# Kernel tuning notes

Measured on AMD Instinct MI355X. Metric: run time of the kernel, lower is better.

## Reference

```python
import jax, jax.numpy as jnp
import numpy as np

# dims: n=batch, T=n_shifts, dX=16, dU=8, H=256 hidden, L=128 ldim, K=64 n_aux (L=2K)

def setup_inputs() -> dict:
    key = jax.random.key(0)
    ks = jax.random.split(key, 16)
    n, T, dX, dU, H, L, K = 64, 64, 16, 8, 256, 128, 64
    def lin(k, fan_in, shape):
        return (jax.random.uniform(k, shape, jnp.float32) * 2.0 - 1.0) / np.sqrt(fan_in)
    xs = jax.random.normal(ks[0], (n, T, dX), jnp.float32)
    us = jax.random.normal(ks[1], (n, T - 1, dU), jnp.float32)
    theta = jax.random.uniform(ks[2], (K,), jnp.float32) * (2.0 * np.pi)
    inp = {
        'xs': xs, 'us': us,
        # stacked x-aux encoders (K copies): BN affine, 3 linear layers (last no bias), output scale
        'x_gamma': jnp.ones((K, dX)), 'x_beta': jnp.zeros((K, dX)),
        'xW1': lin(ks[3], dX, (K, dX, H)), 'xb1': jnp.zeros((K, H)),
        'xW2': lin(ks[4], H, (K, H, H)), 'xb2': jnp.zeros((K, H)),
        'xW3': lin(ks[5], H, (K, H, L)), 'x_scale': jnp.ones((K, L)),
        # stacked u-aux encoders (K copies)
        'u_gamma': jnp.ones((K, dU)), 'u_beta': jnp.zeros((K, dU)),
        'uW1': lin(ks[6], dU, (K, dU, H)), 'ub1': jnp.zeros((K, H)),
        'uW2': lin(ks[7], H, (K, H, H)), 'ub2': jnp.zeros((K, H)),
        'uW3': lin(ks[8], H, (K, H, L)), 'u_scale': jnp.ones((K, L)),
        # Jordan-block complex eigenvalues (|lam| ~ 0.95)
        'reL': 0.95 * jnp.cos(theta), 'imL': 0.95 * jnp.sin(theta),
        # decoder C: Linear(ldim, dim, bias=False) -> weight [dX, L]
        'C_W': lin(ks[9], L, (dX, L)),
    }
    return inp


def _encoder(x, gamma, beta, W1, b1, W2, b2, W3, scale):
    # x: [M, D]; stacked params over K nets. BN stats (training mode) are per-feature over M,
    # identical across nets since the same x feeds every net.
    mu = x.mean(0)
    var = ((x - mu) ** 2).mean(0)
    xn = (x - mu) * jax.lax.rsqrt(var + 1e-5)          # [M, D]
    h = xn[None] * gamma[:, None, :] + beta[:, None, :]  # [K, M, D]
    h = jax.nn.leaky_relu(jnp.einsum('kmd,kdh->kmh', h, W1) + b1[:, None, :])
    h = jax.nn.leaky_relu(jnp.einsum('kmd,kdh->kmh', h, W2) + b2[:, None, :])
    h = jnp.einsum('kmd,kdh->kmh', h, W3)               # last layer: no bias
    return h * scale[:, None, :]                        # [K, M, L]


def reference(xs, us, x_gamma, x_beta, xW1, xb1, xW2, xb2, xW3, x_scale,
              u_gamma, u_beta, uW1, ub1, uW2, ub2, uW3, u_scale, reL, imL, C_W):
    n, T, dX = xs.shape
    K = reL.shape[0]
    L = 2 * K
    Tm1 = T - 1
    # phi1s: [n, T, K(net), K(pair), 2]
    phi = _encoder(xs.reshape(n * T, dX), x_gamma, x_beta, xW1, xb1, xW2, xb2, xW3, x_scale)
    phi1s = jnp.moveaxis(phi, 0, 1).reshape(n, T, K, K, 2)
    # ures = psi(u) - psi(0): [n, T-1, K, K, 2]
    uflat = us.reshape(n * Tm1, -1)
    psi_u = _encoder(uflat, u_gamma, u_beta, uW1, ub1, uW2, ub2, uW3, u_scale)
    psi_0 = _encoder(jnp.zeros_like(uflat), u_gamma, u_beta, uW1, ub1, uW2, ub2, uW3, u_scale)
    ures = jnp.moveaxis(psi_u - psi_0, 0, 1).reshape(n, Tm1, K, K, 2)
    # block-diagonal Koopman: per net j a 2x2 rotation-scale [[re, im], [-im, re]]
    R = jnp.stack([jnp.stack([reL, imL], -1), jnp.stack([-imL, reL], -1)], -2)  # [K, 2, 2]

    def step(p, u_t):
        p = jnp.einsum('bjkc,jcd->bjkd', p + u_t, R)
        return p, p

    _, preds = jax.lax.scan(step, phi1s[:, 0], jnp.moveaxis(ures, 0, 1))
    preds = jnp.moveaxis(preds, 0, 1)  # [n, T-1, K, K, 2]

    def phi2y(p):
        # sum over net axis (-3), flatten pair dims -> [.., L], decode with C
        return p.sum(-3).reshape(*p.shape[:-3], L) @ C_W.T

    y = phi2y(phi1s[:, 1:])
    y_pred = phi2y(preds)
    return y, y_pred
```

## Files before the change

kernel.cpp:

```cpp
#include <hip/hip_runtime.h>

typedef __bf16 bf16_t;
typedef __bf16 bf16x8 __attribute__((ext_vector_type(8)));
typedef __bf16 bf16x4 __attribute__((ext_vector_type(4)));
typedef float  f32x4  __attribute__((ext_vector_type(4)));

__global__ __launch_bounds__(256) void prep_all_kernel(
    const float* __restrict__ xW1, const float* __restrict__ xb1,
    const float* __restrict__ xg,  const float* __restrict__ xbeta,
    const float* __restrict__ uW1, const float* __restrict__ ub1,
    const float* __restrict__ ug,  const float* __restrict__ ubeta,
    const float* __restrict__ xW2, const float* __restrict__ uW2,
    const float* __restrict__ xW3, const float* __restrict__ uW3,
    const float* __restrict__ x_scale, const float* __restrict__ u_scale,
    const float* __restrict__ ub2,
    const float* __restrict__ xs, const float* __restrict__ us,
    bf16_t* __restrict__ xW1t, float* __restrict__ xb1p,
    bf16_t* __restrict__ uW1t, float* __restrict__ ub1p,
    bf16_t* __restrict__ xW2t, bf16_t* __restrict__ uW2t,
    bf16_t* __restrict__ xW3t, bf16_t* __restrict__ uW3t,
    float* __restrict__ psi0, float* __restrict__ part)
{
    const int t = blockIdx.x, tid = threadIdx.x;
    __shared__ float tile[32][65];
    __shared__ float h1[256], h2[256];

    if (t < 6144) {
        const float* in; bf16_t* outp; const float* scale = nullptr;
        int j, r0, c0, C;
        if (t < 4096) {
            C = 256;
            j = (t & 2047) >> 5;
            const int tl = t & 31; r0 = (tl >> 3) * 64; c0 = (tl & 7) * 32;
            if (t < 2048) { in = xW2; outp = xW2t; }
            else          { in = uW2; outp = uW2t; }
        } else {
            C = 128;
            const int l = t - 4096;
            j = (l & 1023) >> 4;
            const int tl = l & 15; r0 = (tl >> 2) * 64; c0 = (tl & 3) * 32;
            if (l < 1024) { in = xW3; outp = xW3t; scale = x_scale + j * 128; }
            else          { in = uW3; outp = uW3t; scale = u_scale + j * 128; }
        }
        in += (size_t)j * 256 * C;
        bf16_t* op = outp + (size_t)j * 256 * C;
        const int cx = tid & 31, ry0 = tid >> 5;
        #pragma unroll
        for (int p = 0; p < 8; p++)
            tile[cx][ry0 + p * 8] = in[(size_t)(r0 + ry0 + p * 8) * C + c0 + cx];
        __syncthreads();
        const int rr = tid & 63, cb = tid >> 6;
        #pragma unroll
        for (int p = 0; p < 8; p++) {
            const int cl = cb + p * 4;
            float sc = scale ? scale[c0 + cl] : 1.f;
            op[(size_t)(c0 + cl) * 256 + r0 + rr] = (bf16_t)(tile[cl][rr] * sc);
        }
    } else if (t < 6272) {
        const int bid = t - 6144, j = bid & 63, h = tid;
        const float *W1, *b1, *gamma, *beta; bf16_t* W1t; float* b1p; int D;
        if (bid < 64) { W1 = xW1; b1 = xb1; gamma = xg; beta = xbeta; W1t = xW1t; b1p = xb1p; D = 16; }
        else          { W1 = uW1; b1 = ub1; gamma = ug; beta = ubeta; W1t = uW1t; b1p = ub1p; D = 8; }
        float bacc = b1[j * 256 + h];
        bf16_t* orow = W1t + (size_t)(j * 256 + h) * 32;
        for (int d = 0; d < 32; d++) orow[d] = (bf16_t)0.f;
        for (int d = 0; d < D; d++) {
            float w = W1[((size_t)j * D + d) * 256 + h];
            orow[d] = (bf16_t)(gamma[j * D + d] * w);
            bacc += beta[j * D + d] * w;
        }
        b1p[j * 256 + h] = bacc;
    } else if (t < 6336) {
        const int j = t - 6272, h = tid;
        {
            float bacc = ub1[j * 256 + h];
            #pragma unroll
            for (int d = 0; d < 8; d++)
                bacc += ubeta[j * 8 + d] * uW1[((size_t)j * 8 + d) * 256 + h];
            h1[h] = fmaxf(bacc, 0.01f * bacc);
        }
        __syncthreads();
        {
            float acc = ub2[j * 256 + h];
            const float* w2 = uW2 + (size_t)j * 65536 + h;
            #pragma unroll 8
            for (int d = 0; d < 256; d++) acc += h1[d] * w2[d * 256];
            h2[h] = fmaxf(acc, 0.01f * acc);
        }
        __syncthreads();
        if (h < 128) {
            float acc = 0.f;
            const float* w3 = uW3 + (size_t)j * 32768 + h;
            #pragma unroll 8
            for (int d = 0; d < 256; d++) acc += h2[d] * w3[d * 128];
            psi0[j * 128 + h] = acc * u_scale[j * 128 + h];
        }
    } else {
        const int bid = t - 6336;
        const bool isx = bid < 64;
        const float* x = isx ? xs : us;
        const int D   = isx ? 16 : 8;
        const int lb  = isx ? bid : bid - 64;
        const int per = isx ? 1024 : 1008;
        const int start = lb * per;
        float a = 0.f, b = 0.f;
        for (int idx = start + tid; idx < start + per; idx += 256) {
            float v = x[idx];
            a += v; b += v * v;
        }
        float* s1 = h1; float* s2 = h2;
        s1[tid] = a; s2[tid] = b;
        __syncthreads();
        if (tid < D) {
            float sa = 0.f, sb = 0.f;
            for (int k = tid; k < 256; k += D) { sa += s1[k]; sb += s2[k]; }
            part[bid * 32 + tid]      = sa;
            part[bid * 32 + 16 + tid] = sb;
        }
    }
}

__global__ __launch_bounds__(512, 4) void fused_mlp_kernel(
    const float* __restrict__ xs, const float* __restrict__ us,
    const float* __restrict__ part,
    const bf16_t* __restrict__ xW1t, const float* __restrict__ xb1p,
    const bf16_t* __restrict__ xW2t, const float* __restrict__ xb2,
    const bf16_t* __restrict__ xW3t,
    const bf16_t* __restrict__ uW1t, const float* __restrict__ ub1p,
    const bf16_t* __restrict__ uW2t, const float* __restrict__ ub2,
    const bf16_t* __restrict__ uW3t,
    bf16_t* __restrict__ phi, bf16_t* __restrict__ psiu)
{
    const int bid  = blockIdx.x;
    const int xcd  = bid & 7;
    const int slot = bid >> 3;
    const int band = slot >> 6;
    const int t64  = slot & 63;
    const int j    = xcd * 8 + band;
    const bool is_x = t64 < 32;
    const int tile  = is_x ? t64 : (t64 - 32);

    const float*  In  = is_x ? xs   : us;
    const int     D   = is_x ? 16   : 8;
    const bf16_t* W1t = is_x ? xW1t : uW1t;
    const float*  b1p = is_x ? xb1p : ub1p;
    const bf16_t* W2t = is_x ? xW2t : uW2t;
    const float*  b2  = is_x ? xb2  : ub2;
    const bf16_t* W3t = is_x ? xW3t : uW3t;
    bf16_t* outp      = is_x ? phi  : psiu;
    const int M       = is_x ? 4096 : 4032;

    const int row0 = tile * 128;
    const int tid  = threadIdx.x;
    const int wave = tid >> 6;
    const int lane = tid & 63;
    const int quad = lane >> 4;
    const int l16  = lane & 15;
    const int lo2  = l16 & 3, hi2 = l16 >> 2;

    __shared__ __align__(16) bf16_t hs[128 * 256];
    __shared__ float stats_s[32];

    if (tid < 16) {
        if (is_x) {
            float sa = 0.f, sb = 0.f;
            #pragma unroll 8
            for (int b = 0; b < 64; b++) { sa += part[b * 32 + tid]; sb += part[b * 32 + 16 + tid]; }
            float mu = sa / 4096.f, var = sb / 4096.f - mu * mu;
            stats_s[tid] = mu; stats_s[16 + tid] = rsqrtf(var + 1e-5f);
        } else if (tid < 8) {
            float sa = 0.f, sb = 0.f;
            #pragma unroll 8
            for (int b = 64; b < 96; b++) { sa += part[b * 32 + tid]; sb += part[b * 32 + 16 + tid]; }
            float mu = sa / 4032.f, var = sb / 4032.f - mu * mu;
            stats_s[tid] = mu; stats_s[16 + tid] = rsqrtf(var + 1e-5f);
        }
    }
    __syncthreads();

    const f32x4 vzero = {0.f, 0.f, 0.f, 0.f};

    char* const hsB = (char*)hs;
    const char* const abase = hsB + l16 * 512 + ((quad ^ lo2) << 4);
    const int  wlow0 = (quad >> 1) ^ lo2;
    char* const wbase = hsB + l16 * 512 + ((wave ^ hi2) << 6) + ((quad & 1) << 3);

    {
        bf16x8 wfr[2];
        #pragma unroll
        for (int nbi = 0; nbi < 2; nbi++)
            wfr[nbi] = *reinterpret_cast<const bf16x8*>(
                W1t + (size_t)(j * 256 + wave * 32 + nbi * 16 + l16) * 32 + quad * 8);

        f32x4 acc[8][2];
        #pragma unroll
        for (int a = 0; a < 8; a++) { acc[a][0] = vzero; acc[a][1] = vzero; }

        const int c0 = quad * 8;
        #pragma unroll
        for (int mb = 0; mb < 8; mb++) {
            bf16x8 a;
            if (c0 < D) {
                int row = row0 + mb * 16 + l16;
                if (row > M - 1) row = M - 1;
                const float* xp = In + (size_t)row * D + c0;
                f32x4 v0 = *reinterpret_cast<const f32x4*>(xp);
                f32x4 v1 = *reinterpret_cast<const f32x4*>(xp + 4);
                #pragma unroll
                for (int e = 0; e < 4; e++) a[e]     = (bf16_t)((v0[e] - stats_s[c0 + e])     * stats_s[16 + c0 + e]);
                #pragma unroll
                for (int e = 0; e < 4; e++) a[4 + e] = (bf16_t)((v1[e] - stats_s[c0 + 4 + e]) * stats_s[16 + c0 + 4 + e]);
            } else {
                #pragma unroll
                for (int e = 0; e < 8; e++) a[e] = (bf16_t)0.f;
            }
            #pragma unroll
            for (int nbi = 0; nbi < 2; nbi++)
                acc[mb][nbi] = __builtin_amdgcn_mfma_f32_16x16x32_bf16(
                    wfr[nbi], a, acc[mb][nbi], 0, 0, 0);
        }

        #pragma unroll
        for (int nbi = 0; nbi < 2; nbi++) {
            const f32x4 bias = *reinterpret_cast<const f32x4*>(
                b1p + j * 256 + wave * 32 + nbi * 16 + quad * 4);
            char* wp = wbase + ((wlow0 ^ (nbi << 1)) << 4);
            #pragma unroll
            for (int mb = 0; mb < 8; mb++) {
                bf16x4 pk;
                #pragma unroll
                for (int r = 0; r < 4; r++) {
                    float v = acc[mb][nbi][r] + bias[r];
                    v = fmaxf(v, 0.01f * v);
                    pk[r] = (bf16_t)v;
                }
                *reinterpret_cast<bf16x4*>(wp + mb * 8192) = pk;
            }
        }
    }
    __syncthreads();

    {
        f32x4 acc[8][2];
        #pragma unroll
        for (int a = 0; a < 8; a++) { acc[a][0] = vzero; acc[a][1] = vzero; }

        const bf16_t* w2base = W2t + ((size_t)j * 256 + wave * 32 + l16) * 256 + quad * 8;

        bf16x8 wr[3][2];
        #pragma unroll
        for (int d = 0; d < 3; d++)
            #pragma unroll
            for (int nbi = 0; nbi < 2; nbi++)
                wr[d][nbi] = *reinterpret_cast<const bf16x8*>(w2base + nbi * 4096 + d * 32);

        #pragma unroll
        for (int kk = 0; kk < 8; kk++) {
            const int c = kk % 3;
            const char* ap = abase + ((kk ^ hi2) << 6);
            bf16x8 av0[4];
            #pragma unroll
            for (int mb = 0; mb < 4; mb++)
                av0[mb] = *reinterpret_cast<const bf16x8*>(ap + mb * 8192);
            #pragma unroll
            for (int nbi = 0; nbi < 2; nbi++)
                #pragma unroll
                for (int mb = 0; mb < 4; mb++)
                    acc[mb][nbi] = __builtin_amdgcn_mfma_f32_16x16x32_bf16(
                        wr[c][nbi], av0[mb], acc[mb][nbi], 0, 0, 0);
            bf16x8 av1[4];
            #pragma unroll
            for (int mb = 0; mb < 4; mb++)
                av1[mb] = *reinterpret_cast<const bf16x8*>(ap + (mb + 4) * 8192);
            #pragma unroll
            for (int nbi = 0; nbi < 2; nbi++)
                #pragma unroll
                for (int mb = 4; mb < 8; mb++)
                    acc[mb][nbi] = __builtin_amdgcn_mfma_f32_16x16x32_bf16(
                        wr[c][nbi], av1[mb - 4], acc[mb][nbi], 0, 0, 0);
            if (kk < 5) {
                #pragma unroll
                for (int nbi = 0; nbi < 2; nbi++)
                    wr[c][nbi] = *reinterpret_cast<const bf16x8*>(
                        w2base + nbi * 4096 + (kk + 3) * 32);
            }
        }
        __syncthreads();
        #pragma unroll
        for (int nbi = 0; nbi < 2; nbi++) {
            const f32x4 bias = *reinterpret_cast<const f32x4*>(
                b2 + j * 256 + wave * 32 + nbi * 16 + quad * 4);
            char* wp = wbase + ((wlow0 ^ (nbi << 1)) << 4);
            #pragma unroll
            for (int mb = 0; mb < 8; mb++) {
                bf16x4 pk;
                #pragma unroll
                for (int r = 0; r < 4; r++) {
                    float v = acc[mb][nbi][r] + bias[r];
                    v = fmaxf(v, 0.01f * v);
                    pk[r] = (bf16_t)v;
                }
                *reinterpret_cast<bf16x4*>(wp + mb * 8192) = pk;
            }
        }
    }
    __syncthreads();

    {
        f32x4 acc[8];
        #pragma unroll
        for (int a = 0; a < 8; a++) acc[a] = vzero;

        const bf16_t* w3base = W3t + ((size_t)j * 128 + wave * 16 + l16) * 256 + quad * 8;

        bf16x8 wr[3];
        #pragma unroll
        for (int d = 0; d < 3; d++)
            wr[d] = *reinterpret_cast<const bf16x8*>(w3base + d * 32);

        #pragma unroll
        for (int kk = 0; kk < 8; kk++) {
            const int c = kk % 3;
            const char* ap = abase + ((kk ^ hi2) << 6);
            bf16x8 av0[4];
            #pragma unroll
            for (int mb = 0; mb < 4; mb++)
                av0[mb] = *reinterpret_cast<const bf16x8*>(ap + mb * 8192);
            #pragma unroll
            for (int mb = 0; mb < 4; mb++)
                acc[mb] = __builtin_amdgcn_mfma_f32_16x16x32_bf16(
                    wr[c], av0[mb], acc[mb], 0, 0, 0);
            bf16x8 av1[4];
            #pragma unroll
            for (int mb = 0; mb < 4; mb++)
                av1[mb] = *reinterpret_cast<const bf16x8*>(ap + (mb + 4) * 8192);
            #pragma unroll
            for (int mb = 4; mb < 8; mb++)
                acc[mb] = __builtin_amdgcn_mfma_f32_16x16x32_bf16(
                    wr[c], av1[mb - 4], acc[mb], 0, 0, 0);
            if (kk < 5)
                wr[c] = *reinterpret_cast<const bf16x8*>(w3base + (kk + 3) * 32);
        }
        __syncthreads();
        {
            const int sp3 = (wave * 2 + (quad >> 1)) ^ l16;
            char* w3p = hsB + l16 * 256 + sp3 * 16 + ((quad & 1) << 3);
            #pragma unroll
            for (int mb = 0; mb < 8; mb++) {
                bf16x4 pk;
                #pragma unroll
                for (int r = 0; r < 4; r++) pk[r] = (bf16_t)acc[mb][r];
                *reinterpret_cast<bf16x4*>(w3p + mb * 4096) = pk;
            }
        }
    }
    __syncthreads();
    #pragma unroll
    for (int p = 0; p < 4; p++) {
        const int rr = p * 32 + (tid >> 4);
        const int s  = tid & 15;
        if (row0 + rr < M) {
            bf16x8 v = *reinterpret_cast<const bf16x8*>(hs + rr * 128 + (s ^ (rr & 15)) * 8);
            *reinterpret_cast<bf16x8*>(outp + ((size_t)j * M + row0 + rr) * 128 + s * 8) = v;
        }
    }
}

__global__ __launch_bounds__(512) void scan_y_kernel(
    const bf16_t* __restrict__ phi, const bf16_t* __restrict__ psiu,
    const float* __restrict__ psi0, const float* __restrict__ reL,
    const float* __restrict__ imL, const float* __restrict__ C_W,
    float* __restrict__ y, float* __restrict__ ypred) {
    const int tid = threadIdx.x;
    __shared__ float Cs[2048];
    __shared__ float red[2][8][128];
    __shared__ float S2[2][128];
    __shared__ float S[32][128];

    #pragma unroll
    for (int i = 0; i < 4; i++) Cs[tid + i * 512] = C_W[tid + i * 512];

    if (blockIdx.x >= 64) {
        const int m0 = (blockIdx.x - 64) * 32;
        const int r  = tid >> 4;
        const int cg = (tid & 15) * 8;
        float acc[8];
        #pragma unroll
        for (int e = 0; e < 8; e++) acc[e] = 0.f;
        const bf16_t* p = phi + (size_t)(m0 + r) * 128 + cg;
        for (int j = 0; j < 64; j += 4) {
            bf16x8 v0 = *reinterpret_cast<const bf16x8*>(p + (size_t)j * 524288);
            bf16x8 v1 = *reinterpret_cast<const bf16x8*>(p + (size_t)(j + 1) * 524288);
            bf16x8 v2 = *reinterpret_cast<const bf16x8*>(p + (size_t)(j + 2) * 524288);
            bf16x8 v3 = *reinterpret_cast<const bf16x8*>(p + (size_t)(j + 3) * 524288);
            #pragma unroll
            for (int e = 0; e < 8; e++)
                acc[e] += (float)v0[e] + (float)v1[e] + (float)v2[e] + (float)v3[e];
        }
        #pragma unroll
        for (int e = 0; e < 8; e++) S[r][cg + e] = acc[e];
        __syncthreads();
        const int mm = tid >> 4, o = tid & 15;
        const int m = m0 + mm;
        if ((m & 63) != 0) {
            float a = 0.f;
            #pragma unroll 8
            for (int l = 0; l < 128; l++) a += S[mm][l] * Cs[o * 128 + l];
            const int b = m >> 6, ti = (m & 63) - 1;
            y[(b * 63 + ti) * 16 + o] = a;
        }
        return;
    }

    const int b = blockIdx.x;
    const int wave = tid >> 6, lane = tid & 63;
    const int j0 = wave * 8;

    float sx[8], sy[8], p0x[8], p0y[8], lre[8], lim[8];
    #pragma unroll
    for (int i = 0; i < 8; i++) {
        const int j = j0 + i;
        unsigned v = *reinterpret_cast<const unsigned*>(
            phi + ((size_t)j * 4096 + b * 64) * 128 + lane * 2);
        sx[i] = __uint_as_float(v << 16);
        sy[i] = __uint_as_float(v & 0xFFFF0000u);
        float2 p0 = *reinterpret_cast<const float2*>(psi0 + j * 128 + lane * 2);
        p0x[i] = p0.x; p0y[i] = p0.y;
        lre[i] = reL[j]; lim[i] = imL[j];
    }
    const bf16_t* upb = psiu + ((size_t)j0 * 4032 + b * 63) * 128 + lane * 2;
    unsigned cur[8];
    #pragma unroll
    for (int i = 0; i < 8; i++)
        cur[i] = *reinterpret_cast<const unsigned*>(upb + (size_t)i * 516096);
    __syncthreads();

    for (int t = 0; t < 63; t++) {
        unsigned nxt[8];
        if (t < 62) {
            #pragma unroll
            for (int i = 0; i < 8; i++)
                nxt[i] = *reinterpret_cast<const unsigned*>(
                    upb + (size_t)i * 516096 + (t + 1) * 128);
        }
        float lsx = 0.f, lsy = 0.f;
        #pragma unroll
        for (int i = 0; i < 8; i++) {
            float px = sx[i] + (__uint_as_float(cur[i] << 16) - p0x[i]);
            float py = sy[i] + (__uint_as_float(cur[i] & 0xFFFF0000u) - p0y[i]);
            sx[i] = px * lre[i] - py * lim[i];
            sy[i] = px * lim[i] + py * lre[i];
            lsx += sx[i]; lsy += sy[i];
        }
        const int db = t & 1;
        red[db][wave][lane * 2]     = lsx;
        red[db][wave][lane * 2 + 1] = lsy;
        __syncthreads();
        if (tid < 128) {
            float s = 0.f;
            #pragma unroll
            for (int w = 0; w < 8; w++) s += red[db][w][tid];
            S2[db][tid] = s;
        }
        __syncthreads();
        if (tid < 128) {
            const int o = tid >> 3, sub = tid & 7;
            float a = 0.f;
            #pragma unroll
            for (int i = 0; i < 16; i++)
                a += S2[db][sub * 16 + i] * Cs[o * 128 + sub * 16 + i];
            a += __shfl_xor(a, 4);
            a += __shfl_xor(a, 2);
            a += __shfl_xor(a, 1);
            if (sub == 0) ypred[(b * 63 + t) * 16 + o] = a;
        }
        #pragma unroll
        for (int i = 0; i < 8; i++) cur[i] = nxt[i];
    }
}

extern "C" void kernel_launch(void* const* d_in, const int* in_sizes, int n_in,
                              void* d_out, int out_size, void* d_ws, size_t ws_size,
                              hipStream_t stream) {
    const float* xs      = (const float*)d_in[0];
    const float* us      = (const float*)d_in[1];
    const float* x_gamma = (const float*)d_in[2];
    const float* x_beta  = (const float*)d_in[3];
    const float* xW1     = (const float*)d_in[4];
    const float* xb1     = (const float*)d_in[5];
    const float* xW2     = (const float*)d_in[6];
    const float* xb2     = (const float*)d_in[7];
    const float* xW3     = (const float*)d_in[8];
    const float* x_scale = (const float*)d_in[9];
    const float* u_gamma = (const float*)d_in[10];
    const float* u_beta  = (const float*)d_in[11];
    const float* uW1     = (const float*)d_in[12];
    const float* ub1     = (const float*)d_in[13];
    const float* uW2     = (const float*)d_in[14];
    const float* ub2     = (const float*)d_in[15];
    const float* uW3     = (const float*)d_in[16];
    const float* u_scale = (const float*)d_in[17];
    const float* reL     = (const float*)d_in[18];
    const float* imL     = (const float*)d_in[19];
    const float* C_W     = (const float*)d_in[20];

    char* ws = (char*)d_ws;
    size_t off = 0;
    auto alloc = [&](size_t bytes) -> char* {
        char* p = ws + off;
        off += (bytes + 255) & ~(size_t)255;
        return p;
    };
    float*  part = (float*)alloc(96 * 32 * 4);
    bf16_t* xW1t = (bf16_t*)alloc((size_t)64 * 256 * 32 * 2);
    float*  xb1p = (float*) alloc((size_t)64 * 256 * 4);
    bf16_t* xW2t = (bf16_t*)alloc((size_t)64 * 256 * 256 * 2);
    bf16_t* xW3t = (bf16_t*)alloc((size_t)64 * 128 * 256 * 2);
    bf16_t* uW1t = (bf16_t*)alloc((size_t)64 * 256 * 32 * 2);
    float*  ub1p = (float*) alloc((size_t)64 * 256 * 4);
    bf16_t* uW2t = (bf16_t*)alloc((size_t)64 * 256 * 256 * 2);
    bf16_t* uW3t = (bf16_t*)alloc((size_t)64 * 128 * 256 * 2);
    float*  psi0 = (float*) alloc((size_t)64 * 128 * 4);
    bf16_t* phi  = (bf16_t*)alloc((size_t)64 * 4096 * 128 * 2);
    bf16_t* psiu = (bf16_t*)alloc((size_t)64 * 4032 * 128 * 2);

    float* y_out     = (float*)d_out;
    float* ypred_out = y_out + 64 * 63 * 16;

    prep_all_kernel<<<6432, 256, 0, stream>>>(
        xW1, xb1, x_gamma, x_beta, uW1, ub1, u_gamma, u_beta,
        xW2, uW2, xW3, uW3, x_scale, u_scale, ub2, xs, us,
        xW1t, xb1p, uW1t, ub1p, xW2t, uW2t, xW3t, uW3t, psi0, part);
    fused_mlp_kernel<<<4096, 512, 0, stream>>>(
        xs, us, part,
        xW1t, xb1p, xW2t, xb2, xW3t, uW1t, ub1p, uW2t, ub2, uW3t, phi, psiu);
    scan_y_kernel<<<192, 512, 0, stream>>>(
        phi, psiu, psi0, reL, imL, C_W, y_out, ypred_out);
}
```

Before: 368.1 us.

## Replace sequential Koopman scan with lower-triangular power-matrix MFMA GEMM

The 63-step sequential recurrence per batch is rewritten as a closed form. Each prediction is a sum of powers of each net's complex eigenvalue times the input terms, so per-net lower-triangular power matrices are precomputed and applied with bf16 MFMA across 512 blocks. The constant psi(0) term is subtracted afterwards using precomputed geometric sums, and a separate decode kernel reduces the 8 net-chunk partials and applies C. This removes the serial 63-step dependency chain and its per-step block syncs, at the cost of an extra kernel, a large fp32 scratch buffer, and bf16 rounding of the eigenvalue powers.

```diff
diff --git a/kernel.cpp b/kernel.cpp
--- a/kernel.cpp
+++ b/kernel.cpp
@@ -3,6 +3,7 @@
 typedef __bf16 bf16_t;
 typedef __bf16 bf16x8 __attribute__((ext_vector_type(8)));
 typedef __bf16 bf16x4 __attribute__((ext_vector_type(4)));
+typedef unsigned short u16x8 __attribute__((ext_vector_type(8)));
 typedef float  f32x4  __attribute__((ext_vector_type(4)));
 
 __global__ __launch_bounds__(256) void prep_all_kernel(
@@ -15,11 +16,13 @@
     const float* __restrict__ x_scale, const float* __restrict__ u_scale,
     const float* __restrict__ ub2,
     const float* __restrict__ xs, const float* __restrict__ us,
+    const float* __restrict__ reL, const float* __restrict__ imL,
     bf16_t* __restrict__ xW1t, float* __restrict__ xb1p,
     bf16_t* __restrict__ uW1t, float* __restrict__ ub1p,
     bf16_t* __restrict__ xW2t, bf16_t* __restrict__ uW2t,
     bf16_t* __restrict__ xW3t, bf16_t* __restrict__ uW3t,
-    float* __restrict__ psi0, float* __restrict__ part)
+    float* __restrict__ psi0, float* __restrict__ part,
+    bf16_t* __restrict__ As, float* __restrict__ sig_re, float* __restrict__ sig_im)
 {
     const int t = blockIdx.x, tid = threadIdx.x;
     __shared__ float tile[32][65];
@@ -95,7 +98,7 @@
             for (int d = 0; d < 256; d++) acc += h2[d] * w3[d * 128];
             psi0[j * 128 + h] = acc * u_scale[j * 128 + h];
         }
-    } else {
+    } else if (t < 6432) {
         const int bid = t - 6336;
         const bool isx = bid < 64;
         const float* x = isx ? xs : us;
@@ -116,6 +119,32 @@
             for (int k = tid; k < 256; k += D) { sa += s1[k]; sb += s2[k]; }
             part[bid * 32 + tid]      = sa;
             part[bid * 32 + 16 + tid] = sb;
+        }
+    } else {
+        const int j = t - 6432;
+        if (tid < 64) {
+            const int r = tid;
+            const float lre = reL[j], lim = imL[j];
+            bf16_t* Ar = As + ((size_t)(j * 2 + 0) * 64 + r) * 64;
+            bf16_t* Ai = As + ((size_t)(j * 2 + 1) * 64 + r) * 64;
+            for (int s = 0; s < 64; s++) { Ar[s] = (bf16_t)0.f; Ai[s] = (bf16_t)0.f; }
+            float px = 1.f, py = 0.f, sre = 0.f, sim = 0.f;
+            for (int k = 1; k <= 64; k++) {
+                const float nx = px * lre - py * lim;
+                py = px * lim + py * lre;
+                px = nx;
+                if (k <= r + 1) {
+                    sre += px; sim += py;
+                    const int col = r + 2 - k;
+                    if (col < 64) {
+                        Ar[col] = (bf16_t)px;
+                        Ai[col] = (bf16_t)py;
+                    }
+                    if (k == r + 1) { Ar[0] = (bf16_t)px; Ai[0] = (bf16_t)py; }
+                }
+            }
+            sig_re[j * 64 + r] = sre;
+            sig_im[j * 64 + r] = sim;
         }
     }
 }
@@ -366,22 +395,96 @@
     }
 }
 
-__global__ __launch_bounds__(512) void scan_y_kernel(
+__global__ __launch_bounds__(256, 2) void scan_gemm_kernel(
     const bf16_t* __restrict__ phi, const bf16_t* __restrict__ psiu,
-    const float* __restrict__ psi0, const float* __restrict__ reL,
-    const float* __restrict__ imL, const float* __restrict__ C_W,
-    float* __restrict__ y, float* __restrict__ ypred) {
+    const bf16_t* __restrict__ As, float* __restrict__ scr)
+{
+    const int b  = blockIdx.x >> 3;
+    const int jc = blockIdx.x & 7;
+    const int tid = threadIdx.x;
+    const int wv  = tid >> 6;
+    const int lane = tid & 63;
+    const int quad = lane >> 4;
+    const int l16  = lane & 15;
+
+    __shared__ unsigned Bt[128 * 52];
+
+    const f32x4 vzero = {0.f, 0.f, 0.f, 0.f};
+    f32x4 accre[8], accim[8];
+    #pragma unroll
+    for (int i = 0; i < 8; i++) { accre[i] = vzero; accim[i] = vzero; }
+
+    const int s2 = tid >> 3;
+    const int c0 = (tid & 7) * 16;
+
+    for (int jj = 0; jj < 8; jj++) {
+        const int j = jc * 8 + jj;
+        const int sA = 2 * s2, sB = 2 * s2 + 1;
+        const bf16_t* rowA = (sA == 0)
+            ? phi  + ((size_t)j * 4096 + b * 64) * 128
+            : psiu + ((size_t)j * 4032 + b * 63 + sA - 1) * 128;
+        const bf16_t* rowB = psiu + ((size_t)j * 4032 + b * 63 + sB - 1) * 128;
+        u16x8 a0 = *reinterpret_cast<const u16x8*>(rowA + c0);
+        u16x8 a1 = *reinterpret_cast<const u16x8*>(rowA + c0 + 8);
+        u16x8 b0 = *reinterpret_cast<const u16x8*>(rowB + c0);
+        u16x8 b1 = *reinterpret_cast<const u16x8*>(rowB + c0 + 8);
+        __syncthreads();
+        #pragma unroll
+        for (int e = 0; e < 8; e++)
+            Bt[(c0 + e) * 52 + s2] = (unsigned)a0[e] | ((unsigned)b0[e] << 16);
+        #pragma unroll
+        for (int e = 0; e < 8; e++)
+            Bt[(c0 + 8 + e) * 52 + s2] = (unsigned)a1[e] | ((unsigned)b1[e] << 16);
+        __syncthreads();
+        #pragma unroll
+        for (int ks = 0; ks < 2; ks++) {
+            bf16x8 Are = *reinterpret_cast<const bf16x8*>(
+                As + ((size_t)(j * 2 + 0) * 64 + wv * 16 + l16) * 64 + ks * 32 + quad * 8);
+            bf16x8 Aim = *reinterpret_cast<const bf16x8*>(
+                As + ((size_t)(j * 2 + 1) * 64 + wv * 16 + l16) * 64 + ks * 32 + quad * 8);
+            #pragma unroll
+            for (int ct = 0; ct < 8; ct++) {
+                bf16x8 Bf = *reinterpret_cast<const bf16x8*>(
+                    &Bt[(ct * 16 + l16) * 52 + ks * 16 + quad * 4]);
+                accre[ct] = __builtin_amdgcn_mfma_f32_16x16x32_bf16(Are, Bf, accre[ct], 0, 0, 0);
+                accim[ct] = __builtin_amdgcn_mfma_f32_16x16x32_bf16(Aim, Bf, accim[ct], 0, 0, 0);
+            }
+        }
+    }
+
+    const float sgn = (l16 & 1) ? 1.f : -1.f;
+    float* out = scr + ((size_t)(b * 8 + jc) * 64) * 128;
+    #pragma unroll
+    for (int ct = 0; ct < 8; ct++) {
+        const int c = ct * 16 + l16;
+        #pragma unroll
+        for (int r = 0; r < 4; r++) {
+            const float vsw = __shfl_xor(accim[ct][r], 1);
+            const int tt = wv * 16 + quad * 4 + r;
+            out[tt * 128 + c] = accre[ct][r] + sgn * vsw;
+        }
+    }
+}
+
+__global__ __launch_bounds__(256) void decode_y_kernel(
+    const bf16_t* __restrict__ phi, const float* __restrict__ scr,
+    const float* __restrict__ psi0,
+    const float* __restrict__ sig_re, const float* __restrict__ sig_im,
+    const float* __restrict__ C_W,
+    float* __restrict__ y, float* __restrict__ ypred)
+{
     const int tid = threadIdx.x;
     __shared__ float Cs[2048];
-    __shared__ float red[2][8][128];
-    __shared__ float S2[2][128];
-    __shared__ float S[32][128];
+    __shared__ float S16[16][128];
+    __shared__ float sigS[2][64][64];
+    __shared__ float psiS[64][128];
+    __shared__ float Sd[64][128];
 
     #pragma unroll
-    for (int i = 0; i < 4; i++) Cs[tid + i * 512] = C_W[tid + i * 512];
-
-    if (blockIdx.x >= 64) {
-        const int m0 = (blockIdx.x - 64) * 32;
+    for (int i = 0; i < 8; i++) Cs[tid + i * 256] = C_W[tid + i * 256];
+
+    if (blockIdx.x < 256) {
+        const int m0 = blockIdx.x * 16;
         const int r  = tid >> 4;
         const int cg = (tid & 15) * 8;
         float acc[8];
@@ -398,84 +501,71 @@
                 acc[e] += (float)v0[e] + (float)v1[e] + (float)v2[e] + (float)v3[e];
         }
         #pragma unroll
-        for (int e = 0; e < 8; e++) S[r][cg + e] = acc[e];
+        for (int e = 0; e < 8; e++) S16[r][cg + e] = acc[e];
         __syncthreads();
         const int mm = tid >> 4, o = tid & 15;
         const int m = m0 + mm;
         if ((m & 63) != 0) {
             float a = 0.f;
             #pragma unroll 8
-            for (int l = 0; l < 128; l++) a += S[mm][l] * Cs[o * 128 + l];
-            const int b = m >> 6, ti = (m & 63) - 1;
-            y[(b * 63 + ti) * 16 + o] = a;
+            for (int l = 0; l < 128; l++) a += S16[mm][l] * Cs[o * 128 + l];
+            const int bb = m >> 6, ti = (m & 63) - 1;
+            y[(bb * 63 + ti) * 16 + o] = a;
         }
         return;
     }
 
-    const int b = blockIdx.x;
-    const int wave = tid >> 6, lane = tid & 63;
-    const int j0 = wave * 8;
-
-    float sx[8], sy[8], p0x[8], p0y[8], lre[8], lim[8];
+    const int b = blockIdx.x - 256;
+    for (int i = tid; i < 4096; i += 256) {
+        ((float*)sigS[0])[i] = sig_re[i];
+        ((float*)sigS[1])[i] = sig_im[i];
+    }
+    for (int i = tid; i < 8192; i += 256) ((float*)psiS)[i] = psi0[i];
+    __syncthreads();
+
+    const int tt = tid >> 2;
+    const int cq = tid & 3;
+    float accv[32];
+    {
+        const float* base = scr + (size_t)(b * 8) * 8192 + tt * 128 + cq * 32;
+        #pragma unroll
+        for (int k = 0; k < 8; k++) {
+            f32x4 s = *reinterpret_cast<const f32x4*>(base + k * 4);
+            #pragma unroll
+            for (int p = 1; p < 8; p++) {
+                f32x4 v = *reinterpret_cast<const f32x4*>(base + (size_t)p * 8192 + k * 4);
+                #pragma unroll
+                for (int e = 0; e < 4; e++) s[e] += v[e];
+            }
+            #pragma unroll
+            for (int e = 0; e < 4; e++) accv[k * 4 + e] = s[e];
+        }
+    }
+    for (int j = 0; j < 64; j++) {
+        const float sr = sigS[0][j][tt];
+        const float si = sigS[1][j][tt];
+        #pragma unroll
+        for (int k = 0; k < 8; k++) {
+            f32x4 pv = *reinterpret_cast<const f32x4*>(&psiS[j][cq * 32 + k * 4]);
+            accv[k * 4 + 0] -= sr * pv[0] - si * pv[1];
+            accv[k * 4 + 1] -= si * pv[0] + sr * pv[1];
+            accv[k * 4 + 2] -= sr * pv[2] - si * pv[3];
+            accv[k * 4 + 3] -= si * pv[2] + sr * pv[3];
+        }
+    }
     #pragma unroll
-    for (int i = 0; i < 8; i++) {
-        const int j = j0 + i;
-        unsigned v = *reinterpret_cast<const unsigned*>(
-            phi + ((size_t)j * 4096 + b * 64) * 128 + lane * 2);
-        sx[i] = __uint_as_float(v << 16);
-        sy[i] = __uint_as_float(v & 0xFFFF0000u);
-        float2 p0 = *reinterpret_cast<const float2*>(psi0 + j * 128 + lane * 2);
-        p0x[i] = p0.x; p0y[i] = p0.y;
-        lre[i] = reL[j]; lim[i] = imL[j];
-    }
-    const bf16_t* upb = psiu + ((size_t)j0 * 4032 + b * 63) * 128 + lane * 2;
-    unsigned cur[8];
+    for (int k = 0; k < 32; k++) Sd[tt][cq * 32 + k] = accv[k];
+    __syncthreads();
     #pragma unroll
-    for (int i = 0; i < 8; i++)
-        cur[i] = *reinterpret_cast<const unsigned*>(upb + (size_t)i * 516096);
-    __syncthreads();
-
-    for (int t = 0; t < 63; t++) {
-        unsigned nxt[8];
-        if (t < 62) {
-            #pragma unroll
-            for (int i = 0; i < 8; i++)
-                nxt[i] = *reinterpret_cast<const unsigned*>(
-                    upb + (size_t)i * 516096 + (t + 1) * 128);
-        }
-        float lsx = 0.f, lsy = 0.f;
-        #pragma unroll
-        for (int i = 0; i < 8; i++) {
-            float px = sx[i] + (__uint_as_float(cur[i] << 16) - p0x[i]);
-            float py = sy[i] + (__uint_as_float(cur[i] & 0xFFFF0000u) - p0y[i]);
-            sx[i] = px * lre[i] - py * lim[i];
-            sy[i] = px * lim[i] + py * lre[i];
-            lsx += sx[i]; lsy += sy[i];
-        }
-        const int db = t & 1;
-        red[db][wave][lane * 2]     = lsx;
-        red[db][wave][lane * 2 + 1] = lsy;
-        __syncthreads();
-        if (tid < 128) {
-            float s = 0.f;
-            #pragma unroll
-            for (int w = 0; w < 8; w++) s += red[db][w][tid];
-            S2[db][tid] = s;
-        }
-        __syncthreads();
-        if (tid < 128) {
-            const int o = tid >> 3, sub = tid & 7;
+    for (int i = 0; i < 4; i++) {
+        const int idx = tid + i * 256;
+        if (idx < 1008) {
+            const int t = idx >> 4, o = idx & 15;
             float a = 0.f;
-            #pragma unroll
-            for (int i = 0; i < 16; i++)
-                a += S2[db][sub * 16 + i] * Cs[o * 128 + sub * 16 + i];
-            a += __shfl_xor(a, 4);
-            a += __shfl_xor(a, 2);
-            a += __shfl_xor(a, 1);
-            if (sub == 0) ypred[(b * 63 + t) * 16 + o] = a;
-        }
-        #pragma unroll
-        for (int i = 0; i < 8; i++) cur[i] = nxt[i];
+            #pragma unroll 8
+            for (int l = 0; l < 128; l++) a += Sd[t][l] * Cs[o * 128 + l];
+            ypred[(b * 63 + t) * 16 + o] = a;
+        }
     }
 }
 
@@ -521,19 +611,25 @@
     bf16_t* uW2t = (bf16_t*)alloc((size_t)64 * 256 * 256 * 2);
     bf16_t* uW3t = (bf16_t*)alloc((size_t)64 * 128 * 256 * 2);
     float*  psi0 = (float*) alloc((size_t)64 * 128 * 4);
+    bf16_t* As   = (bf16_t*)alloc((size_t)64 * 2 * 64 * 64 * 2);
+    float*  sigr = (float*) alloc((size_t)64 * 64 * 4);
+    float*  sigi = (float*) alloc((size_t)64 * 64 * 4);
     bf16_t* phi  = (bf16_t*)alloc((size_t)64 * 4096 * 128 * 2);
     bf16_t* psiu = (bf16_t*)alloc((size_t)64 * 4032 * 128 * 2);
+    float*  scr  = (float*) alloc((size_t)64 * 8 * 64 * 128 * 4);
 
     float* y_out     = (float*)d_out;
     float* ypred_out = y_out + 64 * 63 * 16;
 
-    prep_all_kernel<<<6432, 256, 0, stream>>>(
+    prep_all_kernel<<<6496, 256, 0, stream>>>(
         xW1, xb1, x_gamma, x_beta, uW1, ub1, u_gamma, u_beta,
-        xW2, uW2, xW3, uW3, x_scale, u_scale, ub2, xs, us,
-        xW1t, xb1p, uW1t, ub1p, xW2t, uW2t, xW3t, uW3t, psi0, part);
+        xW2, uW2, xW3, uW3, x_scale, u_scale, ub2, xs, us, reL, imL,
+        xW1t, xb1p, uW1t, ub1p, xW2t, uW2t, xW3t, uW3t, psi0, part,
+        As, sigr, sigi);
     fused_mlp_kernel<<<4096, 512, 0, stream>>>(
         xs, us, part,
         xW1t, xb1p, xW2t, xb2, xW3t, uW1t, ub1p, uW2t, ub2, uW3t, phi, psiu);
-    scan_y_kernel<<<192, 512, 0, stream>>>(
-        phi, psiu, psi0, reL, imL, C_W, y_out, ypred_out);
+    scan_gemm_kernel<<<512, 256, 0, stream>>>(phi, psiu, As, scr);
+    decode_y_kernel<<<320, 256, 0, stream>>>(
+        phi, scr, psi0, sigr, sigi, C_W, y_out, ypred_out);
 }
```

Result: slower. 390.8 us (+6.2%).
